# Kernel optimization log

Hardware: AMD Instinct MI355X
Metric: run time of the kernel (lower is better)

Reference implementation:

```python
import jax, jax.numpy as jnp
import numpy as np

IMG = 224; P = 16; C_IN = 3; D = 768; DEPTH = 12; H = 12; HD = D // H
MLP = 4 * D; NCLS = 1000
GRID = IMG // P; NPATCH = GRID * GRID; N = NPATCH + 1
NRD = (2 * GRID - 1) * (2 * GRID - 1) + 3  # num_relative_distance


def _rel_pos_index():
    # replicates the torch buffer construction (BEiT-style)
    coords = np.stack(np.meshgrid(np.arange(GRID), np.arange(GRID), indexing='ij')).reshape(2, -1)
    rel = (coords[:, :, None] - coords[:, None, :]).transpose(1, 2, 0).astype(np.int64)
    rel[:, :, 0] += GRID - 1
    rel[:, :, 1] += GRID - 1
    rel[:, :, 0] *= 2 * GRID - 1
    idx = np.zeros((N, N), dtype=np.int64)
    idx[1:, 1:] = rel.sum(-1)
    idx[0, :] = NRD - 3
    idx[:, 0] = NRD - 2
    idx[0, 0] = NRD - 1
    return jnp.asarray(idx)

REL_IDX = _rel_pos_index()  # [N, N] int


def setup_inputs() -> dict:
    key = jax.random.key(0)
    ks = jax.random.split(key, 12)
    r = lambda k, shp: jax.random.normal(k, shp, jnp.float32) * 0.02
    return {
        'x': jax.random.normal(ks[0], (32, C_IN, IMG, IMG), jnp.float32),
        'patch_w': r(ks[1], (D, C_IN * P * P)),
        'patch_b': jnp.zeros((D,), jnp.float32),
        'cls_token': r(ks[2], (1, 1, D)),
        'pos_embed': r(ks[3], (1, N, D)),
        'norm1_s': jnp.ones((DEPTH, D), jnp.float32),
        'norm1_b': jnp.zeros((DEPTH, D), jnp.float32),
        'qkv_w': r(ks[4], (DEPTH, 3 * D, D)),
        'q_bias': jnp.zeros((DEPTH, D), jnp.float32),
        'v_bias': jnp.zeros((DEPTH, D), jnp.float32),
        'rpb_table': r(ks[5], (DEPTH, NRD, H)),
        'proj_w': r(ks[6], (DEPTH, D, D)),
        'proj_b': jnp.zeros((DEPTH, D), jnp.float32),
        'norm2_s': jnp.ones((DEPTH, D), jnp.float32),
        'norm2_b': jnp.zeros((DEPTH, D), jnp.float32),
        'fc1_w': r(ks[7], (DEPTH, MLP, D)),
        'fc1_b': jnp.zeros((DEPTH, MLP), jnp.float32),
        'fc2_w': r(ks[8], (DEPTH, D, MLP)),
        'fc2_b': jnp.zeros((DEPTH, D), jnp.float32),
        'gamma1': jnp.full((DEPTH, D), 0.1, jnp.float32),
        'gamma2': jnp.full((DEPTH, D), 0.1, jnp.float32),
        'normf_s': jnp.ones((D,), jnp.float32),
        'normf_b': jnp.zeros((D,), jnp.float32),
        'head_w': r(ks[9], (NCLS, D)),
        'head_b': jnp.zeros((NCLS,), jnp.float32),
    }


def _ln(x, s, b):
    m = jnp.mean(x, -1, keepdims=True)
    v = jnp.mean((x - m) ** 2, -1, keepdims=True)
    return (x - m) * jax.lax.rsqrt(v + 1e-5) * s + b


def reference(x, patch_w, patch_b, cls_token, pos_embed, norm1_s, norm1_b, qkv_w,
              q_bias, v_bias, rpb_table, proj_w, proj_b, norm2_s, norm2_b,
              fc1_w, fc1_b, fc2_w, fc2_b, gamma1, gamma2, normf_s, normf_b,
              head_w, head_b):
    B = x.shape[0]
    # Patch embed: stride=kernel conv == unfold + matmul
    t = x.reshape(B, C_IN, GRID, P, GRID, P).transpose(0, 2, 4, 1, 3, 5).reshape(B, NPATCH, C_IN * P * P)
    t = t @ patch_w.T + patch_b                                   # [B, 196, D]
    t = jnp.concatenate([jnp.broadcast_to(cls_token, (B, 1, D)), t], axis=1) + pos_embed
    scale = HD ** -0.5
    for i in range(DEPTH):
        h = _ln(t, norm1_s[i], norm1_b[i])
        qkv_b = jnp.concatenate([q_bias[i], jnp.zeros_like(q_bias[i]), v_bias[i]])
        qkv = (h @ qkv_w[i].T + qkv_b).reshape(B, N, 3, H, HD)
        q = qkv[:, :, 0].transpose(0, 2, 1, 3)                    # [B, H, N, HD]
        k = qkv[:, :, 1].transpose(0, 2, 1, 3)
        v = qkv[:, :, 2].transpose(0, 2, 1, 3)
        bias = rpb_table[i][REL_IDX].transpose(2, 0, 1)           # [H, N, N]
        attn = jax.nn.softmax(jnp.einsum('bhqd,bhkd->bhqk', q * scale, k) + bias[None], axis=-1)
        o = jnp.einsum('bhqk,bhkd->bhqd', attn, v).transpose(0, 2, 1, 3).reshape(B, N, D)
        t = t + gamma1[i] * (o @ proj_w[i].T + proj_b[i])
        h2 = _ln(t, norm2_s[i], norm2_b[i])
        m = jax.nn.gelu(h2 @ fc1_w[i].T + fc1_b[i], approximate=False) @ fc2_w[i].T + fc2_b[i]
        t = t + gamma2[i] * m
    t = _ln(t, normf_s, normf_b)
    return t[:, 0] @ head_w.T + head_b                            # [B, NCLS]
```

## Files before the change

kernel.cpp:

```cpp
#include <hip/hip_runtime.h>
#include <hip/hip_bf16.h>


typedef __hip_bfloat16 bf16s;
using bf16x8 = __attribute__((ext_vector_type(8))) __bf16;
using f32x4  = __attribute__((ext_vector_type(4))) float;

#define DEV static __device__ __forceinline__

DEV float b2f(bf16s x) { return __bfloat162float(x); }
DEV bf16s f2b(float x) { return __float2bfloat16(x); }

DEV void gload_lds16(const void* g, void* l) {
  __builtin_amdgcn_global_load_lds((const __attribute__((address_space(1))) void*)g,
                                   (__attribute__((address_space(3))) void*)l, 16, 0, 0);
}

constexpr int B_   = 32;
constexpr int H_   = 12;
constexpr int NTOK = 197;
constexpr int NPAD = 224;
constexpr int MVALP= 6272;
constexpr int MVAL = B_*NTOK;
constexpr int MROW = 6400;
constexpr int MLP_ = 3072;
constexpr int BH   = B_*H_;
constexpr int NRD  = 732;
constexpr int NN   = NTOK*NTOK;

constexpr size_t OFF_T   = 0;
constexpr size_t SZ_T    = (size_t)MROW*768*4;
constexpr size_t OFF_H   = OFF_T + SZ_T;
constexpr size_t SZ_H    = (size_t)MROW*768*2;
constexpr size_t OFF_Q   = OFF_H + SZ_H;
constexpr size_t SZ_QKB  = (size_t)BH*NPAD*64*2;
constexpr size_t OFF_K   = OFF_Q + SZ_QKB;
constexpr size_t OFF_VT  = OFF_K + SZ_QKB;
constexpr size_t OFF_P   = OFF_VT + SZ_QKB;
constexpr size_t SZ_P    = (size_t)MROW*MLP_*2;
constexpr size_t OFF_O   = OFF_P + SZ_P;
constexpr size_t OFF_BT  = OFF_O + SZ_H;
constexpr size_t SZ_BT   = (size_t)12*H_*NN*2;
constexpr size_t OFF_HF  = OFF_BT + SZ_BT;
constexpr size_t OFF_WB  = OFF_HF + 49152;
constexpr size_t WS_NEED = OFF_WB + (size_t)7077888*2;

constexpr size_t WB_QKV = 0;
constexpr size_t WB_PROJ= (size_t)2304*768;
constexpr size_t WB_FC1 = WB_PROJ + (size_t)768*768;
constexpr size_t WB_FC2 = WB_FC1 + (size_t)MLP_*768;

template<int MODE>
__global__ __launch_bounds__(512, 4)
void gemm8p(const bf16s* __restrict__ A, const bf16s* __restrict__ Bw,
            const int K, const int ldc,
            bf16s* __restrict__ Cb,
            const float* __restrict__ e0, const float* __restrict__ e1,
            float* __restrict__ tres,
            bf16s* __restrict__ qp, bf16s* __restrict__ kp, bf16s* __restrict__ vp)
{
  __shared__ bf16s lds[32768];
  const int tid  = threadIdx.x;
  const int lane = tid & 63;
  const int wid  = tid >> 6;
  const int wm   = wid >> 2, wn = wid & 3;

  const int ncols = gridDim.y;
  const int nwg = (int)gridDim.x * ncols;
  const int lin = (int)blockIdx.y * gridDim.x + blockIdx.x;
  const int xcd = lin & 7, pos = lin >> 3;
  const int q8 = nwg >> 3, r8 = nwg & 7;
  const int vid = (xcd < r8) ? xcd*(q8+1) + pos : r8*(q8+1) + (xcd-r8)*q8 + pos;

  int bm, bn, koff = 0, ksl = 0;
  if (MODE == 6) {
    ksl = vid / 300;
    const int rem = vid - ksl*300;
    bm = rem / 6; bn = rem - bm*6;
    koff = ksl * 768;
  } else {
    constexpr int NBG = (MODE == 0) ? 6 : 8;
    const int gsz = NBG * (int)gridDim.x;
    const int g   = vid / gsz;
    const int rr  = vid - g*gsz;
    bm  = rr / NBG;
    bn  = g*NBG + (rr - bm*NBG);
  }

  const int ldk = (MODE == 6) ? ldc : K;
  const int srow = (wid << 3) + (lane >> 3);
  const int colg = ((lane & 7) << 3) ^ (((srow >> 2) & 1) << 4);
  const bf16s* gA = A  + (size_t)(bm*128 + srow)*ldk + koff + colg;
  const bf16s* gB = Bw + (size_t)(bn*128 + srow)*ldk + koff + colg;
  const size_t rK64 = (size_t)64*ldk;

  const int r15  = lane & 15;
  const int colr = (lane >> 4) << 3;
  const int cxor = ((lane >> 2) & 1) << 4;
  const int ardA = wm*4096 + r15*64;
  const int ardB = 8192 + (wn*32 + r15)*64;

  f32x4 acc[4][2] = {};
  const int J = K >> 7;

#define STGA(h, kt, dbuf) do { \
    const bf16s* _g = gA + (size_t)(h)*rK64 + (size_t)(kt)*64; \
    gload_lds16(_g, &lds[(dbuf)*16384 + (h)*4096 + wid*512 + lane*8]); } while(0)
#define STGB(h, kt, dbuf) do { \
    const bf16s* _g = gB + (size_t)(h)*rK64 + (size_t)(kt)*64; \
    gload_lds16(_g, &lds[(dbuf)*16384 + 8192 + (h)*4096 + wid*512 + lane*8]); } while(0)

  STGB(0,0,0); STGB(1,0,0);
  STGA(0,0,0); STGA(1,0,0);
  STGB(0,1,1); STGB(1,1,1);

  bf16x8 bfr[2][2];

  for (int j = 0; j < J; ++j) {
    const bool more = (j+1 < J);
#pragma unroll
    for (int p = 0; p < 4; ++p) {
      __builtin_amdgcn_sched_barrier(0);
      if (p == 0) {
        asm volatile("s_waitcnt vmcnt(2)" ::: "memory");
      } else if (p == 2) {
        if (j+1 == J) asm volatile("s_waitcnt vmcnt(0)" ::: "memory");
        else          asm volatile("s_waitcnt vmcnt(2)" ::: "memory");
      }
      __builtin_amdgcn_sched_barrier(0);
      __builtin_amdgcn_s_barrier();
      __builtin_amdgcn_sched_barrier(0);

      if (p == 0)      { STGA(0, 2*j+1, 1); STGA(1, 2*j+1, 1); }
      else if (p == 1) { if (more) { STGB(0, 2*j+2, 0); STGB(1, 2*j+2, 0); } }
      else if (p == 2) { if (more) { STGA(0, 2*j+2, 0); STGA(1, 2*j+2, 0); } }
      else             { if (more) { STGB(0, 2*j+3, 1); STGB(1, 2*j+3, 1); } }

      const int d = (p < 2) ? 0 : 1;
      const int dbase = d*16384;
      const int q0 = (p & 1) << 1;
      if ((p & 1) == 0) {
#pragma unroll
        for (int nf=0; nf<2; nf++)
#pragma unroll
          for (int kss=0; kss<2; kss++)
            bfr[nf][kss] = *(const bf16x8*)&lds[dbase + ardB + nf*1024 + (((kss<<5) + colr) ^ cxor)];
      }
      bf16x8 a1[2][2];
#pragma unroll
      for (int qq=0; qq<2; qq++)
#pragma unroll
        for (int kss=0; kss<2; kss++)
          a1[qq][kss] = *(const bf16x8*)&lds[dbase + ardA + (q0+qq)*1024 + (((kss<<5) + colr) ^ cxor)];
      __builtin_amdgcn_s_setprio(1);
#pragma unroll
      for (int qq=0; qq<2; qq++)
#pragma unroll
        for (int nf=0; nf<2; nf++)
#pragma unroll
          for (int kss=0; kss<2; kss++)
            acc[q0+qq][nf] = __builtin_amdgcn_mfma_f32_16x16x32_bf16(a1[qq][kss], bfr[nf][kss], acc[q0+qq][nf], 0, 0, 0);
      __builtin_amdgcn_s_setprio(0);
    }
  }
#undef STGA
#undef STGB

  const int crow0 = (lane >> 4) * 4;

  if (MODE == 6) {
#pragma unroll
    for (int mf = 0; mf < 4; ++mf) {
#pragma unroll
      for (int r = 0; r < 4; ++r) {
        const int grow = bm*128 + wm*64 + mf*16 + crow0 + r;
        float* trow = tres + (size_t)grow*768;
#pragma unroll
        for (int nf = 0; nf < 2; ++nf) {
          const int gcol = bn*128 + wn*32 + nf*16 + r15;
          const float add = e1[gcol]*(acc[mf][nf][r] + ((ksl == 0) ? e0[gcol] : 0.0f));
          unsafeAtomicAdd(&trow[gcol], add);
        }
      }
    }
    return;
  }

  if (MODE == 5) {
#pragma unroll
    for (int mf = 0; mf < 4; ++mf) {
#pragma unroll
      for (int r = 0; r < 4; ++r) {
        const int grow = bm*128 + wm*64 + mf*16 + crow0 + r;
        bf16s* crow = Cb + (size_t)grow*ldc;
#pragma unroll
        for (int nf = 0; nf < 2; ++nf) {
          const int gcol = bn*128 + wn*32 + nf*16 + r15;
          const float xx = acc[mf][nf][r] + e0[gcol];
          crow[gcol] = f2b(0.5f*xx*(1.0f + erff(xx*0.70710678118654752f)));
        }
      }
    }
    return;
  }

  if (MODE == 0 && bn >= 12) {
    float* lf = (float*)lds;
    __syncthreads();
#pragma unroll
    for (int mf = 0; mf < 4; ++mf)
#pragma unroll
      for (int nf = 0; nf < 2; ++nf)
#pragma unroll
        for (int r = 0; r < 4; ++r) {
          const int col = wn*32 + nf*16 + r15;
          const int row = wm*64 + mf*16 + crow0 + r;
          lf[col*128 + (row ^ (col & 31))] = acc[mf][nf][r];
        }
    __syncthreads();
    const int rem0 = bn*128 - 1536;
#pragma unroll
    for (int ci = 0; ci < 16; ++ci) {
      const int c = wid*16 + ci;
      const int rem = rem0 + c;
      const int hh = rem >> 6, dd = rem & 63;
      const float vb = e1[rem];
      bf16s* vrow = vp + ((size_t)hh*64 + dd)*NPAD;
#pragma unroll
      for (int hf2 = 0; hf2 < 2; ++hf2) {
        const int row = hf2*64 + lane;
        const int grow = bm*128 + row;
        if (grow < MVAL) {
          const int b2 = grow/197, ntok = grow - b2*197;
          vrow[(size_t)b2*H_*64*NPAD + ntok] = f2b(lf[c*128 + (row ^ (c & 31))] + vb);
        }
      }
    }
    return;
  }

  if (MODE == 0) {
#pragma unroll
    for (int mf = 0; mf < 4; ++mf) {
#pragma unroll
      for (int r = 0; r < 4; ++r) {
        const int grow = bm*128 + wm*64 + mf*16 + crow0 + r;
        if (grow >= MVAL) continue;
        const int bb_ = grow/197, ntok = grow - bb_*197;
#pragma unroll
        for (int nf = 0; nf < 2; ++nf) {
          const int gcol = bn*128 + wn*32 + nf*16 + r15;
          const float v = acc[mf][nf][r];
          const int rem = (gcol >= 768) ? gcol-768 : gcol;
          const int hh = rem >> 6, dd = rem & 63;
          const size_t bh = (size_t)bb_*H_ + hh;
          if (gcol < 768) qp[(bh*NPAD + ntok)*64 + dd] = f2b((v + e0[rem])*0.125f);
          else            kp[(bh*NPAD + ntok)*64 + dd] = f2b(v);
        }
      }
    }
  }
}

template<int MODE>
__global__ __launch_bounds__(256, 3)
void gemm64n(const bf16s* __restrict__ A, const bf16s* __restrict__ Bw,
             const int K, const int ldc, bf16s* __restrict__ Cb,
             const float* __restrict__ e0, const float* __restrict__ e1,
             float* __restrict__ tres)
{
  __shared__ bf16s lds[24576];
  const int tid  = threadIdx.x;
  const int lane = tid & 63;
  const int wid  = tid >> 6;
  const int wm   = wid >> 1, wn = wid & 1;

  const int ncols = gridDim.y;
  const int nwg = (int)gridDim.x * ncols;
  const int lin = (int)blockIdx.y * gridDim.x + blockIdx.x;
  const int xcd = lin & 7, pos = lin >> 3;
  const int q8 = nwg >> 3, r8 = nwg & 7;
  const int vid = (xcd < r8) ? xcd*(q8+1) + pos : r8*(q8+1) + (xcd-r8)*q8 + pos;
  const int bm = vid / ncols, bn = vid - bm*ncols;

  const int srow = tid >> 3;
  const int colg = ((tid & 7) << 3) ^ (((srow >> 2) & 1) << 4);
  const bf16s* gA = A  + (size_t)(bm*128 + srow)*K + colg;
  const bf16s* gB = Bw + (size_t)(bn*64  + srow)*K + colg;
  const size_t rK32 = (size_t)32*K;

  const int r15  = lane & 15;
  const int colr = (lane >> 4) << 3;
  const int cxor = ((lane >> 2) & 1) << 4;
  const int ardA = wm*4096 + r15*64;
  const int ardB = 8192 + (wn*32 + r15)*64;

  f32x4 acc[4][2] = {};
  const int J = K >> 7;

#define STGA2(h, kt, dbuf) do { \
    const bf16s* _g = gA + (size_t)(h)*rK32 + (size_t)(kt)*64; \
    gload_lds16(_g, &lds[(dbuf)*12288 + (h)*2048 + tid*8]); } while(0)
#define STGB2(h, kt, dbuf) do { \
    const bf16s* _g = gB + (size_t)(h)*rK32 + (size_t)(kt)*64; \
    gload_lds16(_g, &lds[(dbuf)*12288 + 8192 + (h)*2048 + tid*8]); } while(0)

  STGB2(0,0,0); STGB2(1,0,0);
  STGA2(0,0,0); STGA2(1,0,0); STGA2(2,0,0); STGA2(3,0,0);
  STGB2(0,1,1); STGB2(1,1,1);

  bf16x8 bfr[2][2];

  for (int j = 0; j < J; ++j) {
    const bool more = (j+1 < J);
#pragma unroll
    for (int p = 0; p < 4; ++p) {
      __builtin_amdgcn_sched_barrier(0);
      if (p == 0) {
        asm volatile("s_waitcnt vmcnt(2)" ::: "memory");
      } else if (p == 2) {
        if (j+1 == J) asm volatile("s_waitcnt vmcnt(0)" ::: "memory");
        else          asm volatile("s_waitcnt vmcnt(2)" ::: "memory");
      }
      __builtin_amdgcn_sched_barrier(0);
      __builtin_amdgcn_s_barrier();
      __builtin_amdgcn_sched_barrier(0);

      if (p == 0)      { STGA2(0, 2*j+1, 1); STGA2(1, 2*j+1, 1); STGA2(2, 2*j+1, 1); STGA2(3, 2*j+1, 1); }
      else if (p == 1) { if (more) { STGB2(0, 2*j+2, 0); STGB2(1, 2*j+2, 0); } }
      else if (p == 2) { if (more) { STGA2(0, 2*j+2, 0); STGA2(1, 2*j+2, 0); STGA2(2, 2*j+2, 0); STGA2(3, 2*j+2, 0); } }
      else             { if (more) { STGB2(0, 2*j+3, 1); STGB2(1, 2*j+3, 1); } }

      const int d = (p < 2) ? 0 : 1;
      const int dbase = d*12288;
      const int q0 = (p & 1) << 1;
      if ((p & 1) == 0) {
#pragma unroll
        for (int nf=0; nf<2; nf++)
#pragma unroll
          for (int kss=0; kss<2; kss++)
            bfr[nf][kss] = *(const bf16x8*)&lds[dbase + ardB + nf*1024 + (((kss<<5) + colr) ^ cxor)];
      }
      bf16x8 a1[2][2];
#pragma unroll
      for (int qq=0; qq<2; qq++)
#pragma unroll
        for (int kss=0; kss<2; kss++)
          a1[qq][kss] = *(const bf16x8*)&lds[dbase + ardA + (q0+qq)*1024 + (((kss<<5) + colr) ^ cxor)];
      __builtin_amdgcn_s_setprio(1);
#pragma unroll
      for (int qq=0; qq<2; qq++)
#pragma unroll
        for (int nf=0; nf<2; nf++)
#pragma unroll
          for (int kss=0; kss<2; kss++)
            acc[q0+qq][nf] = __builtin_amdgcn_mfma_f32_16x16x32_bf16(a1[qq][kss], bfr[nf][kss], acc[q0+qq][nf], 0, 0, 0);
      __builtin_amdgcn_s_setprio(0);
    }
  }
#undef STGA2
#undef STGB2

  const int crow0 = (lane >> 4) * 4;
#pragma unroll
  for (int mf = 0; mf < 4; ++mf) {
#pragma unroll
    for (int r = 0; r < 4; ++r) {
      const int grow = bm*128 + wm*64 + mf*16 + crow0 + r;
      if (MODE == 3) {
        bf16s* crow = Cb + (size_t)grow*ldc;
#pragma unroll
        for (int nf = 0; nf < 2; ++nf) {
          const int gcol = bn*64 + wn*32 + nf*16 + r15;
          const float xx = acc[mf][nf][r] + e0[gcol];
          crow[gcol] = f2b(0.5f*xx*(1.0f + erff(xx*0.70710678118654752f)));
        }
      } else {
        float* trow = tres + (size_t)grow*768;
#pragma unroll
        for (int nf = 0; nf < 2; ++nf) {
          const int gcol = bn*64 + wn*32 + nf*16 + r15;
          trow[gcol] += e1[gcol]*(acc[mf][nf][r] + e0[gcol]);
        }
      }
    }
  }
}

__global__ __launch_bounds__(256, 5)
void gemm64p(const bf16s* __restrict__ A, const bf16s* __restrict__ Bw,
             int K,
             const float* __restrict__ e0, const float* __restrict__ e1,
             float* __restrict__ tres)
{
  __shared__ bf16s As[2][64*32];
  __shared__ bf16s Bs[2][128*32];
  const int tid  = threadIdx.x;
  const int lane = tid & 63;
  const int wave = tid >> 6;

  const int ncols = gridDim.y;
  const int nwg = (int)gridDim.x * ncols;
  const int lin = (int)blockIdx.y * gridDim.x + blockIdx.x;
  const int xcd = lin & 7, pos = lin >> 3;
  const int q8 = nwg >> 3, r8 = nwg & 7;
  const int vid = (xcd < r8) ? xcd*(q8+1) + pos : r8*(q8+1) + (xcd-r8)*q8 + pos;
  const int bm = vid / ncols, bn = vid - bm*ncols;

  f32x4 acc[2][4] = {};

  const int sr4  = lane >> 2;
  const int scol = ((lane&3) ^ (sr4&3))*8;
  const bf16s* gA = A  + (size_t)(bm*64  + wave*16 + sr4)*K + scol;
  const bf16s* gB = Bw + (size_t)(bn*128 + wave*32 + sr4)*K + scol;
  const size_t b16 = (size_t)16*K;
  const int dA  = wave*512  + lane*8;
  const int dB0 = wave*1024 + lane*8, dB1 = dB0 + 512;

  const int fr  = lane & 15;
  const int rdk = (((lane>>4) ^ (lane&3)))*8;
  const int wr = wave >> 1, wc = wave & 1;
  const int abase = (wr*32 + fr)*32 + rdk;
  const int bbase = (wc*64 + fr)*32 + rdk;

  const int nk = K >> 5;
  gload_lds16(gA,       &As[0][dA]);
  gload_lds16(gB,       &Bs[0][dB0]);
  gload_lds16(gB + b16, &Bs[0][dB1]);

  int cur = 0;
  for (int kt = 0; kt < nk; ++kt) {
    __syncthreads();
    if (kt + 1 < nk) {
      const bf16s* ga = gA + (size_t)(kt+1)*32;
      const bf16s* gb = gB + (size_t)(kt+1)*32;
      gload_lds16(ga,       &As[cur^1][dA]);
      gload_lds16(gb,       &Bs[cur^1][dB0]);
      gload_lds16(gb + b16, &Bs[cur^1][dB1]);
    }
    bf16x8 af[2], bfr[4];
    af[0] = *(const bf16x8*)&As[cur][abase];
    af[1] = *(const bf16x8*)&As[cur][abase + 512];
#pragma unroll
    for (int n2=0;n2<4;n2++) bfr[n2] = *(const bf16x8*)&Bs[cur][bbase + n2*512];
#pragma unroll
    for (int m=0;m<2;m++)
#pragma unroll
      for (int n2=0;n2<4;n2++)
        acc[m][n2] = __builtin_amdgcn_mfma_f32_16x16x32_bf16(af[m], bfr[n2], acc[m][n2], 0, 0, 0);
    cur ^= 1;
  }

  const int crow0 = (lane>>4)*4;
#pragma unroll
  for (int m=0;m<2;m++) {
#pragma unroll
    for (int r=0;r<4;r++) {
      const int grow = bm*64 + wr*32 + m*16 + crow0 + r;
      if (grow >= MVALP) continue;
      const int bb_ = grow/196, p = grow - bb_*196;
      float* trow = tres + ((size_t)bb_*197 + 1 + p)*768;
      const float* prow = e1 + (size_t)(1+p)*768;
#pragma unroll
      for (int n2=0;n2<4;n2++) {
        const int gcol = bn*128 + wc*64 + n2*16 + fr;
        trow[gcol] = acc[m][n2][r] + e0[gcol] + prow[gcol];
      }
    }
  }
}

__global__ __launch_bounds__(256)
void f2b_k(const float* __restrict__ src, bf16s* __restrict__ dst, int n4)
{
  int id = blockIdx.x*256 + threadIdx.x;
  if (id >= n4) return;
  const float4 v = ((const float4*)src)[id];
  union { bf16s b[4]; uint2 u; } uu;
  uu.b[0] = f2b(v.x); uu.b[1] = f2b(v.y); uu.b[2] = f2b(v.z); uu.b[3] = f2b(v.w);
  ((uint2*)dst)[id] = uu.u;
}

__global__ __launch_bounds__(256)
void prep_k(const float* __restrict__ tin, const float* __restrict__ s,
            const float* __restrict__ b, bf16s* __restrict__ outp,
            const float* __restrict__ qw, const float* __restrict__ pw,
            const float* __restrict__ f1, const float* __restrict__ f2,
            bf16s* __restrict__ wb)
{
  const int tid = threadIdx.x;
  if (blockIdx.x < MVAL) {
    const int r = blockIdx.x;
    const float* xr = tin + (size_t)r*768;
    float v0 = xr[tid], v1 = xr[tid+256], v2 = xr[tid+512];
    float sum = v0+v1+v2;
#pragma unroll
    for (int off=32; off>=1; off>>=1) sum += __shfl_xor(sum, off, 64);
    __shared__ float red[8];
    const int wv = tid>>6, ln = tid&63;
    if (ln==0) red[wv] = sum;
    __syncthreads();
    const float mean = (red[0]+red[1]+red[2]+red[3]) * (1.0f/768.0f);
    const float d0=v0-mean, d1=v1-mean, d2=v2-mean;
    float sq = d0*d0 + d1*d1 + d2*d2;
#pragma unroll
    for (int off=32; off>=1; off>>=1) sq += __shfl_xor(sq, off, 64);
    if (ln==0) red[4+wv] = sq;
    __syncthreads();
    const float rs = rsqrtf((red[4]+red[5]+red[6]+red[7])*(1.0f/768.0f) + 1e-5f);
    bf16s* orow = outp + (size_t)r*768;
    orow[tid]     = f2b(d0*rs*s[tid]     + b[tid]);
    orow[tid+256] = f2b(d1*rs*s[tid+256] + b[tid+256]);
    orow[tid+512] = f2b(d2*rs*s[tid+512] + b[tid+512]);
  } else {
    int id = (blockIdx.x - MVAL)*256 + tid;
    const float* src; size_t dst; int loc;
    if (id < 442368)           { src = qw; loc = id;          dst = WB_QKV; }
    else if (id < 589824)      { src = pw; loc = id-442368;   dst = WB_PROJ; }
    else if (id < 1179648)     { src = f1; loc = id-589824;   dst = WB_FC1; }
    else                       { src = f2; loc = id-1179648;  dst = WB_FC2; }
    const float4 v = ((const float4*)src)[loc];
    union { bf16s bb[4]; uint2 u; } uu;
    uu.bb[0] = f2b(v.x); uu.bb[1] = f2b(v.y); uu.bb[2] = f2b(v.z); uu.bb[3] = f2b(v.w);
    ((uint2*)(wb + dst))[loc] = uu.u;
  }
}

__global__ __launch_bounds__(256)
void bias_all_k(const float* __restrict__ rpb, bf16s* __restrict__ biasT)
{
  int id = blockIdx.x*256 + threadIdx.x;
  if (id >= 12*H_*NN) return;
  const int l   = id / (H_*NN);
  const int r2  = id - l*(H_*NN);
  const int hh  = r2 / NN;
  const int rem = r2 - hh*NN;
  const int i = rem / 197, j = rem - i*197;
  int v;
  if (i==0 && j==0)      v = NRD-1;
  else if (i==0)         v = NRD-3;
  else if (j==0)         v = NRD-2;
  else {
    const int p = i-1, q = j-1;
    v = (p/14 - q/14 + 13)*27 + (p%14 - q%14 + 13);
  }
  biasT[id] = f2b(rpb[(size_t)l*NRD*H_ + v*H_ + hh]);
}

__global__ __launch_bounds__(256)
void im2col_k(const float* __restrict__ x, bf16s* __restrict__ pat)
{
  int id = blockIdx.x*256 + threadIdx.x;
  if (id >= MVALP*768) return;
  int col = id % 768;  int row = id / 768;
  int b = row / 196, p = row % 196;
  int gy = p / 14, gx = p % 14;
  int c = col >> 8, rem = col & 255, py = rem >> 4, px = rem & 15;
  pat[id] = f2b(x[ ((size_t)(b*3 + c)*224 + gy*16 + py)*224 + gx*16 + px ]);
}

__global__ __launch_bounds__(256)
void clspos_k(const float* __restrict__ cls, const float* __restrict__ pos, float* __restrict__ t)
{
  int id = blockIdx.x*256 + threadIdx.x;
  int d = id % 768, b = id / 768;
  t[(size_t)b*197*768 + d] = cls[d] + pos[d];
}

__global__ __launch_bounds__(256)
void ln_k(const float* __restrict__ tin, const float* __restrict__ s,
          const float* __restrict__ b, bf16s* __restrict__ outp, int instride)
{
  const int r = blockIdx.x, tid = threadIdx.x;
  const float* xr = tin + (size_t)r*instride;
  float v0 = xr[tid], v1 = xr[tid+256], v2 = xr[tid+512];
  float sum = v0+v1+v2;
#pragma unroll
  for (int off=32; off>=1; off>>=1) sum += __shfl_xor(sum, off, 64);
  __shared__ float red[8];
  const int wv = tid>>6, ln = tid&63;
  if (ln==0) red[wv] = sum;
  __syncthreads();
  const float mean = (red[0]+red[1]+red[2]+red[3]) * (1.0f/768.0f);
  const float d0=v0-mean, d1=v1-mean, d2=v2-mean;
  float sq = d0*d0 + d1*d1 + d2*d2;
#pragma unroll
  for (int off=32; off>=1; off>>=1) sq += __shfl_xor(sq, off, 64);
  if (ln==0) red[4+wv] = sq;
  __syncthreads();
  const float rs = rsqrtf((red[4]+red[5]+red[6]+red[7])*(1.0f/768.0f) + 1e-5f);
  bf16s* orow = outp + (size_t)r*768;
  orow[tid]     = f2b(d0*rs*s[tid]     + b[tid]);
  orow[tid+256] = f2b(d1*rs*s[tid+256] + b[tid+256]);
  orow[tid+512] = f2b(d2*rs*s[tid+512] + b[tid+512]);
}

__global__ __launch_bounds__(64)
void attn_fused(const bf16s* __restrict__ q, const bf16s* __restrict__ k,
                const bf16s* __restrict__ vT, const bf16s* __restrict__ biasT,
                bf16s* __restrict__ o)
{
  __shared__ bf16s Pl[32][232];
  const int gid = blockIdx.x;
  const int qt = gid % 7, bh = gid / 7;
  const int b = bh / H_, hh = bh % H_;
  const int lane = threadIdx.x;
  const int fr = lane & 15, fk = (lane>>4)*8;
  const bf16s* qp = q + (size_t)bh*NPAD*64;
  const bf16s* kp = k + (size_t)bh*NPAD*64;
  bf16x8 a[2][2];
#pragma unroll
  for (int m=0;m<2;m++)
#pragma unroll
    for (int kk=0;kk<2;kk++)
      a[m][kk] = *(const bf16x8*)&qp[(qt*32 + m*16 + fr)*64 + kk*32 + fk];

  f32x4 acc[2][14] = {};
#pragma unroll
  for (int nt=0; nt<14; nt++) {
    bf16x8 bb0 = *(const bf16x8*)&kp[(nt*16 + fr)*64 + fk];
    bf16x8 bb1 = *(const bf16x8*)&kp[(nt*16 + fr)*64 + 32 + fk];
    acc[0][nt] = __builtin_amdgcn_mfma_f32_16x16x32_bf16(a[0][0], bb0, acc[0][nt], 0,0,0);
    acc[0][nt] = __builtin_amdgcn_mfma_f32_16x16x32_bf16(a[0][1], bb1, acc[0][nt], 0,0,0);
    acc[1][nt] = __builtin_amdgcn_mfma_f32_16x16x32_bf16(a[1][0], bb0, acc[1][nt], 0,0,0);
    acc[1][nt] = __builtin_amdgcn_mfma_f32_16x16x32_bf16(a[1][1], bb1, acc[1][nt], 0,0,0);
  }

  const bf16s* bT = biasT + (size_t)hh*NN;
#pragma unroll
  for (int m=0;m<2;m++) {
#pragma unroll
    for (int r2=0;r2<4;r2++) {
      const int lrow = m*16 + (lane>>4)*4 + r2;
      const int row = qt*32 + lrow;
      if (row < NTOK) {
        const bf16s* br = bT + (size_t)row*197;
        float s[14]; float mx = -3.0e38f;
#pragma unroll
        for (int nt=0; nt<14; nt++) {
          const int col = nt*16 + fr;
          float v = acc[m][nt][r2] + ((col < NTOK) ? b2f(br[col]) : 0.0f);
          s[nt] = v;
          if (col < NTOK) mx = fmaxf(mx, v);
        }
        mx = fmaxf(mx, __shfl_xor(mx, 1, 64));
        mx = fmaxf(mx, __shfl_xor(mx, 2, 64));
        mx = fmaxf(mx, __shfl_xor(mx, 4, 64));
        mx = fmaxf(mx, __shfl_xor(mx, 8, 64));
        float sum = 0.f;
#pragma unroll
        for (int nt=0; nt<14; nt++) {
          const int col = nt*16 + fr;
          float p = (col < NTOK) ? __expf(s[nt]-mx) : 0.0f;
          s[nt] = p; sum += p;
        }
        sum += __shfl_xor(sum, 1, 64);
        sum += __shfl_xor(sum, 2, 64);
        sum += __shfl_xor(sum, 4, 64);
        sum += __shfl_xor(sum, 8, 64);
        const float inv = 1.0f / sum;
#pragma unroll
        for (int nt=0; nt<14; nt++)
          Pl[lrow][nt*16 + fr] = f2b(s[nt]*inv);
      } else {
#pragma unroll
        for (int nt=0; nt<14; nt++)
          Pl[lrow][nt*16 + fr] = f2b(0.0f);
      }
    }
  }

  __syncthreads();

  const bf16s* Vp = vT + (size_t)bh*64*NPAD;
  f32x4 pacc[2][4] = {};
  for (int kt=0; kt<7; kt++) {
    bf16x8 a0 = *(const bf16x8*)&Pl[fr][kt*32 + fk];
    bf16x8 a1 = *(const bf16x8*)&Pl[16 + fr][kt*32 + fk];
#pragma unroll
    for (int nf=0;nf<4;nf++) {
      bf16x8 bb = *(const bf16x8*)&Vp[(size_t)(nf*16 + fr)*NPAD + kt*32 + fk];
      pacc[0][nf] = __builtin_amdgcn_mfma_f32_16x16x32_bf16(a0, bb, pacc[0][nf], 0,0,0);
      pacc[1][nf] = __builtin_amdgcn_mfma_f32_16x16x32_bf16(a1, bb, pacc[1][nf], 0,0,0);
    }
  }

  __syncthreads();
#pragma unroll
  for (int m=0;m<2;m++)
#pragma unroll
    for (int nf=0;nf<4;nf++)
#pragma unroll
      for (int r2=0;r2<4;r2++)
        Pl[m*16 + (lane>>4)*4 + r2][nf*16 + fr] = f2b(pacc[m][nf][r2]);
  __syncthreads();
  bf16s* obase = o + ((size_t)b*NTOK + qt*32)*768 + hh*64;
#pragma unroll
  for (int it=0; it<8; ++it) {
    const int id = it*64 + lane;
    const int row = id >> 4, c4 = (id & 15)*4;
    if (qt*32 + row < NTOK) {
      union { bf16s bb[4]; uint2 u; } uu;
      uu.bb[0]=Pl[row][c4]; uu.bb[1]=Pl[row][c4+1]; uu.bb[2]=Pl[row][c4+2]; uu.bb[3]=Pl[row][c4+3];
      *(uint2*)&obase[(size_t)row*768 + c4] = uu.u;
    }
  }
}

__global__ __launch_bounds__(256)
void head_k(const bf16s* __restrict__ hf, const float* __restrict__ hw,
            const float* __restrict__ hb, float* __restrict__ outp)
{
  const int b = blockIdx.y;
  const int n = blockIdx.x*256 + threadIdx.x;
  __shared__ float xs[768];
  for (int i=threadIdx.x; i<768; i+=256) xs[i] = b2f(hf[b*768+i]);
  __syncthreads();
  if (n < 1000) {
    const float* wr = hw + (size_t)n*768;
    float acc2 = hb[n];
    for (int k2=0;k2<768;k2++) acc2 += xs[k2]*wr[k2];
    outp[b*1000 + n] = acc2;
  }
}

extern "C" void kernel_launch(void* const* d_in, const int* in_sizes, int n_in,
                              void* d_out, int out_size, void* d_ws, size_t ws_size,
                              hipStream_t stream)
{
  const float* x       = (const float*)d_in[0];
  const float* patch_w = (const float*)d_in[1];
  const float* patch_b = (const float*)d_in[2];
  const float* cls_tok = (const float*)d_in[3];
  const float* pos_emb = (const float*)d_in[4];
  const float* norm1_s = (const float*)d_in[5];
  const float* norm1_b = (const float*)d_in[6];
  const float* qkv_w   = (const float*)d_in[7];
  const float* q_bias  = (const float*)d_in[8];
  const float* v_bias  = (const float*)d_in[9];
  const float* rpb     = (const float*)d_in[10];
  const float* proj_w  = (const float*)d_in[11];
  const float* proj_b  = (const float*)d_in[12];
  const float* norm2_s = (const float*)d_in[13];
  const float* norm2_b = (const float*)d_in[14];
  const float* fc1_w   = (const float*)d_in[15];
  const float* fc1_b   = (const float*)d_in[16];
  const float* fc2_w   = (const float*)d_in[17];
  const float* fc2_b   = (const float*)d_in[18];
  const float* gamma1  = (const float*)d_in[19];
  const float* gamma2  = (const float*)d_in[20];
  const float* normf_s = (const float*)d_in[21];
  const float* normf_b = (const float*)d_in[22];
  const float* head_w  = (const float*)d_in[23];
  const float* head_b  = (const float*)d_in[24];
  float* out = (float*)d_out;

  char* w = (char*)d_ws;
  float* t    = (float*)(w + OFF_T);
  bf16s* h    = (bf16s*)(w + OFF_H);
  bf16s* qb   = (bf16s*)(w + OFF_Q);
  bf16s* kb   = (bf16s*)(w + OFF_K);
  bf16s* vT   = (bf16s*)(w + OFF_VT);
  bf16s* m1   = (bf16s*)(w + OFF_P);
  bf16s* pat  = (bf16s*)(w + OFF_P);
  bf16s* o    = (bf16s*)(w + OFF_O);
  bf16s* biasT= (bf16s*)(w + OFF_BT);
  bf16s* hf   = (bf16s*)(w + OFF_HF);
  bf16s* wb   = (bf16s*)(w + OFF_WB);
  (void)ws_size; (void)in_sizes; (void)n_in; (void)out_size; (void)WS_NEED;

  hipMemsetAsync(h  + (size_t)MVAL*768,  0, (size_t)(MROW-MVAL)*768*2,  stream);
  hipMemsetAsync(o  + (size_t)MVAL*768,  0, (size_t)(MROW-MVAL)*768*2,  stream);
  hipMemsetAsync(m1 + (size_t)MVAL*MLP_, 0, (size_t)(MROW-MVAL)*MLP_*2, stream);
  hipMemsetAsync(qb, 0, SZ_QKB, stream);
  hipMemsetAsync(kb, 0, SZ_QKB, stream);
  hipMemsetAsync(vT, 0, SZ_QKB, stream);

  bias_all_k<<<(12*H_*NN + 255)/256, 256, 0, stream>>>(rpb, biasT);
  im2col_k<<<(MVALP*768)/256, 256, 0, stream>>>(x, pat);
  clspos_k<<<96, 256, 0, stream>>>(cls_tok, pos_emb, t);
  f2b_k<<<(768*768/4)/256, 256, 0, stream>>>(patch_w, wb, 768*768/4);
  gemm64p<<<dim3(98,6), 256, 0, stream>>>(pat, wb, 768, patch_b, pos_emb, t);

  for (int l = 0; l < 12; ++l) {
    prep_k<<<MVAL + 6912, 256, 0, stream>>>(t, norm1_s + l*768, norm1_b + l*768, h,
                                            qkv_w + (size_t)l*2304*768, proj_w + (size_t)l*768*768,
                                            fc1_w + (size_t)l*MLP_*768, fc2_w + (size_t)l*768*MLP_, wb);
    gemm8p<0><<<dim3(50,18), 512, 0, stream>>>(h, wb + WB_QKV, 768, 2304, nullptr,
                                               q_bias + l*768, v_bias + l*768, nullptr,
                                               qb, kb, vT);
    attn_fused<<<BH*7, 64, 0, stream>>>(qb, kb, vT, biasT + (size_t)l*H_*NN, o);
    gemm64n<2><<<dim3(50,12), 256, 0, stream>>>(o, wb + WB_PROJ, 768, 0, nullptr,
                                                proj_b + l*768, gamma1 + l*768, t);
    ln_k<<<MVAL, 256, 0, stream>>>(t, norm2_s + l*768, norm2_b + l*768, h, 768);
    gemm8p<5><<<dim3(50,24), 512, 0, stream>>>(h, wb + WB_FC1, 768, MLP_, m1,
                                               fc1_b + l*MLP_, nullptr, nullptr,
                                               nullptr, nullptr, nullptr);
    gemm8p<6><<<dim3(50,24), 512, 0, stream>>>(m1, wb + WB_FC2, 768, MLP_, nullptr,
                                               fc2_b + l*768, gamma2 + l*768, t,
                                               nullptr, nullptr, nullptr);
  }

  ln_k<<<32, 256, 0, stream>>>(t, normf_s, normf_b, hf, 197*768);
  head_k<<<dim3(4,32), 256, 0, stream>>>(hf, head_w, head_b, out);
}
```

Before: 3.272 ms.

## Replace FC2 split-K atomics with partial buffers reduced in next LayerNorm

The FC2 split-K GEMM no longer does atomic adds into the residual stream. Each K-slice now writes plain fp32 partials into a 4-slice buffer, and the next layer's prep_k (or the final LayerNorm) sums the partials, applies bias and gamma2, and updates the residual. This removes atomic contention in the FC2 epilogue at the cost of extra global traffic for writing and reading four partial planes. Separately, the LDS XOR swizzle changes from a 1-bit pattern to a full 3-bit row-based swizzle to cut bank conflicts, and a dead MODE 3 epilogue branch is removed.

Measured after the change: 2.898 ms. 1.13x faster.

```diff
diff --git a/kernel.cpp b/kernel.cpp
--- a/kernel.cpp
+++ b/kernel.cpp
@@ -43,7 +43,12 @@
 constexpr size_t SZ_BT   = (size_t)12*H_*NN*2;
 constexpr size_t OFF_HF  = OFF_BT + SZ_BT;
 constexpr size_t OFF_WB  = OFF_HF + 49152;
-constexpr size_t WS_NEED = OFF_WB + (size_t)7077888*2;
+constexpr size_t SZ_WB   = (size_t)7077888*2;
+constexpr size_t OFF_PK  = OFF_WB + SZ_WB;
+constexpr size_t SZ_PK   = (size_t)4*MROW*768*4;
+constexpr size_t WS_NEED = OFF_PK + SZ_PK;
+
+constexpr size_t PST = (size_t)MROW*768;
 
 constexpr size_t WB_QKV = 0;
 constexpr size_t WB_PROJ= (size_t)2304*768;
@@ -89,14 +94,14 @@
 
   const int ldk = (MODE == 6) ? ldc : K;
   const int srow = (wid << 3) + (lane >> 3);
-  const int colg = ((lane & 7) << 3) ^ (((srow >> 2) & 1) << 4);
+  const int colg = (((lane & 7) ^ (srow & 7)) << 3);
   const bf16s* gA = A  + (size_t)(bm*128 + srow)*ldk + koff + colg;
   const bf16s* gB = Bw + (size_t)(bn*128 + srow)*ldk + koff + colg;
   const size_t rK64 = (size_t)64*ldk;
 
   const int r15  = lane & 15;
   const int colr = (lane >> 4) << 3;
-  const int cxor = ((lane >> 2) & 1) << 4;
+  const int exor = (lane & 7) << 3;
   const int ardA = wm*4096 + r15*64;
   const int ardB = 8192 + (wn*32 + r15)*64;
 
@@ -144,14 +149,14 @@
         for (int nf=0; nf<2; nf++)
 #pragma unroll
           for (int kss=0; kss<2; kss++)
-            bfr[nf][kss] = *(const bf16x8*)&lds[dbase + ardB + nf*1024 + (((kss<<5) + colr) ^ cxor)];
+            bfr[nf][kss] = *(const bf16x8*)&lds[dbase + ardB + nf*1024 + (((kss<<5) + colr) ^ exor)];
       }
       bf16x8 a1[2][2];
 #pragma unroll
       for (int qq=0; qq<2; qq++)
 #pragma unroll
         for (int kss=0; kss<2; kss++)
-          a1[qq][kss] = *(const bf16x8*)&lds[dbase + ardA + (q0+qq)*1024 + (((kss<<5) + colr) ^ cxor)];
+          a1[qq][kss] = *(const bf16x8*)&lds[dbase + ardA + (q0+qq)*1024 + (((kss<<5) + colr) ^ exor)];
       __builtin_amdgcn_s_setprio(1);
 #pragma unroll
       for (int qq=0; qq<2; qq++)
@@ -169,17 +174,17 @@
   const int crow0 = (lane >> 4) * 4;
 
   if (MODE == 6) {
+    float* pb = tres + (size_t)ksl*PST;
 #pragma unroll
     for (int mf = 0; mf < 4; ++mf) {
 #pragma unroll
       for (int r = 0; r < 4; ++r) {
         const int grow = bm*128 + wm*64 + mf*16 + crow0 + r;
-        float* trow = tres + (size_t)grow*768;
+        float* prow = pb + (size_t)grow*768;
 #pragma unroll
         for (int nf = 0; nf < 2; ++nf) {
           const int gcol = bn*128 + wn*32 + nf*16 + r15;
-          const float add = e1[gcol]*(acc[mf][nf][r] + ((ksl == 0) ? e0[gcol] : 0.0f));
-          unsafeAtomicAdd(&trow[gcol], add);
+          prow[gcol] = acc[mf][nf][r];
         }
       }
     }
@@ -284,14 +289,14 @@
   const int bm = vid / ncols, bn = vid - bm*ncols;
 
   const int srow = tid >> 3;
-  const int colg = ((tid & 7) << 3) ^ (((srow >> 2) & 1) << 4);
+  const int colg = (((tid & 7) ^ (srow & 7)) << 3);
   const bf16s* gA = A  + (size_t)(bm*128 + srow)*K + colg;
   const bf16s* gB = Bw + (size_t)(bn*64  + srow)*K + colg;
   const size_t rK32 = (size_t)32*K;
 
   const int r15  = lane & 15;
   const int colr = (lane >> 4) << 3;
-  const int cxor = ((lane >> 2) & 1) << 4;
+  const int exor = (lane & 7) << 3;
   const int ardA = wm*4096 + r15*64;
   const int ardB = 8192 + (wn*32 + r15)*64;
 
@@ -339,14 +344,14 @@
         for (int nf=0; nf<2; nf++)
 #pragma unroll
           for (int kss=0; kss<2; kss++)
-            bfr[nf][kss] = *(const bf16x8*)&lds[dbase + ardB + nf*1024 + (((kss<<5) + colr) ^ cxor)];
+            bfr[nf][kss] = *(const bf16x8*)&lds[dbase + ardB + nf*1024 + (((kss<<5) + colr) ^ exor)];
       }
       bf16x8 a1[2][2];
 #pragma unroll
       for (int qq=0; qq<2; qq++)
 #pragma unroll
         for (int kss=0; kss<2; kss++)
-          a1[qq][kss] = *(const bf16x8*)&lds[dbase + ardA + (q0+qq)*1024 + (((kss<<5) + colr) ^ cxor)];
+          a1[qq][kss] = *(const bf16x8*)&lds[dbase + ardA + (q0+qq)*1024 + (((kss<<5) + colr) ^ exor)];
       __builtin_amdgcn_s_setprio(1);
 #pragma unroll
       for (int qq=0; qq<2; qq++)
@@ -367,15 +372,7 @@
 #pragma unroll
     for (int r = 0; r < 4; ++r) {
       const int grow = bm*128 + wm*64 + mf*16 + crow0 + r;
-      if (MODE == 3) {
-        bf16s* crow = Cb + (size_t)grow*ldc;
-#pragma unroll
-        for (int nf = 0; nf < 2; ++nf) {
-          const int gcol = bn*64 + wn*32 + nf*16 + r15;
-          const float xx = acc[mf][nf][r] + e0[gcol];
-          crow[gcol] = f2b(0.5f*xx*(1.0f + erff(xx*0.70710678118654752f)));
-        }
-      } else {
+      {
         float* trow = tres + (size_t)grow*768;
 #pragma unroll
         for (int nf = 0; nf < 2; ++nf) {
@@ -482,17 +479,29 @@
 }
 
 __global__ __launch_bounds__(256)
-void prep_k(const float* __restrict__ tin, const float* __restrict__ s,
+void prep_k(float* __restrict__ tio, const float* __restrict__ s,
             const float* __restrict__ b, bf16s* __restrict__ outp,
             const float* __restrict__ qw, const float* __restrict__ pw,
             const float* __restrict__ f1, const float* __restrict__ f2,
-            bf16s* __restrict__ wb)
+            bf16s* __restrict__ wb,
+            const float* __restrict__ pk, const float* __restrict__ g2,
+            const float* __restrict__ b2)
 {
   const int tid = threadIdx.x;
   if (blockIdx.x < MVAL) {
     const int r = blockIdx.x;
-    const float* xr = tin + (size_t)r*768;
+    float* xr = tio + (size_t)r*768;
     float v0 = xr[tid], v1 = xr[tid+256], v2 = xr[tid+512];
+    if (pk) {
+      const size_t base = (size_t)r*768;
+      const float p0 = pk[base+tid]     + pk[PST+base+tid]     + pk[2*PST+base+tid]     + pk[3*PST+base+tid];
+      const float p1 = pk[base+tid+256] + pk[PST+base+tid+256] + pk[2*PST+base+tid+256] + pk[3*PST+base+tid+256];
+      const float p2 = pk[base+tid+512] + pk[PST+base+tid+512] + pk[2*PST+base+tid+512] + pk[3*PST+base+tid+512];
+      v0 += g2[tid]    *(p0 + b2[tid]);
+      v1 += g2[tid+256]*(p1 + b2[tid+256]);
+      v2 += g2[tid+512]*(p2 + b2[tid+512]);
+      xr[tid] = v0; xr[tid+256] = v1; xr[tid+512] = v2;
+    }
     float sum = v0+v1+v2;
 #pragma unroll
     for (int off=32; off>=1; off>>=1) sum += __shfl_xor(sum, off, 64);
@@ -569,11 +578,24 @@
 
 __global__ __launch_bounds__(256)
 void ln_k(const float* __restrict__ tin, const float* __restrict__ s,
-          const float* __restrict__ b, bf16s* __restrict__ outp, int instride)
+          const float* __restrict__ b, bf16s* __restrict__ outp, int instride,
+          const float* __restrict__ pk, const float* __restrict__ g2,
+          const float* __restrict__ b2)
 {
   const int r = blockIdx.x, tid = threadIdx.x;
   const float* xr = tin + (size_t)r*instride;
   float v0 = xr[tid], v1 = xr[tid+256], v2 = xr[tid+512];
+  if (pk) {
+    const size_t base = (size_t)r*(size_t)instride;
+    const size_t bp = (size_t)r*197*768;
+    const float p0 = pk[bp+tid]     + pk[PST+bp+tid]     + pk[2*PST+bp+tid]     + pk[3*PST+bp+tid];
+    const float p1 = pk[bp+tid+256] + pk[PST+bp+tid+256] + pk[2*PST+bp+tid+256] + pk[3*PST+bp+tid+256];
+    const float p2 = pk[bp+tid+512] + pk[PST+bp+tid+512] + pk[2*PST+bp+tid+512] + pk[3*PST+bp+tid+512];
+    v0 += g2[tid]    *(p0 + b2[tid]);
+    v1 += g2[tid+256]*(p1 + b2[tid+256]);
+    v2 += g2[tid+512]*(p2 + b2[tid+512]);
+    (void)base;
+  }
   float sum = v0+v1+v2;
 #pragma unroll
   for (int off=32; off>=1; off>>=1) sum += __shfl_xor(sum, off, 64);
@@ -767,6 +789,7 @@
   bf16s* biasT= (bf16s*)(w + OFF_BT);
   bf16s* hf   = (bf16s*)(w + OFF_HF);
   bf16s* wb   = (bf16s*)(w + OFF_WB);
+  float* pbuf = (float*)(w + OFF_PK);
   (void)ws_size; (void)in_sizes; (void)n_in; (void)out_size; (void)WS_NEED;
 
   hipMemsetAsync(h  + (size_t)MVAL*768,  0, (size_t)(MROW-MVAL)*768*2,  stream);
@@ -783,24 +806,30 @@
   gemm64p<<<dim3(98,6), 256, 0, stream>>>(pat, wb, 768, patch_b, pos_emb, t);
 
   for (int l = 0; l < 12; ++l) {
+    const float* pkin = (l > 0) ? pbuf : nullptr;
+    const float* g2in = (l > 0) ? gamma2 + (l-1)*768 : nullptr;
+    const float* b2in = (l > 0) ? fc2_b  + (l-1)*768 : nullptr;
     prep_k<<<MVAL + 6912, 256, 0, stream>>>(t, norm1_s + l*768, norm1_b + l*768, h,
                                             qkv_w + (size_t)l*2304*768, proj_w + (size_t)l*768*768,
-                                            fc1_w + (size_t)l*MLP_*768, fc2_w + (size_t)l*768*MLP_, wb);
+                                            fc1_w + (size_t)l*MLP_*768, fc2_w + (size_t)l*768*MLP_, wb,
+                                            pkin, g2in, b2in);
     gemm8p<0><<<dim3(50,18), 512, 0, stream>>>(h, wb + WB_QKV, 768, 2304, nullptr,
                                                q_bias + l*768, v_bias + l*768, nullptr,
                                                qb, kb, vT);
     attn_fused<<<BH*7, 64, 0, stream>>>(qb, kb, vT, biasT + (size_t)l*H_*NN, o);
     gemm64n<2><<<dim3(50,12), 256, 0, stream>>>(o, wb + WB_PROJ, 768, 0, nullptr,
                                                 proj_b + l*768, gamma1 + l*768, t);
-    ln_k<<<MVAL, 256, 0, stream>>>(t, norm2_s + l*768, norm2_b + l*768, h, 768);
+    ln_k<<<MVAL, 256, 0, stream>>>(t, norm2_s + l*768, norm2_b + l*768, h, 768,
+                                   nullptr, nullptr, nullptr);
     gemm8p<5><<<dim3(50,24), 512, 0, stream>>>(h, wb + WB_FC1, 768, MLP_, m1,
                                                fc1_b + l*MLP_, nullptr, nullptr,
                                                nullptr, nullptr, nullptr);
     gemm8p<6><<<dim3(50,24), 512, 0, stream>>>(m1, wb + WB_FC2, 768, MLP_, nullptr,
-                                               fc2_b + l*768, gamma2 + l*768, t,
+                                               nullptr, nullptr, pbuf,
                                                nullptr, nullptr, nullptr);
   }
 
-  ln_k<<<32, 256, 0, stream>>>(t, normf_s, normf_b, hf, 197*768);
+  ln_k<<<32, 256, 0, stream>>>(t, normf_s, normf_b, hf, 197*768,
+                               pbuf, gamma2 + 11*768, fc2_b + 11*768);
   head_k<<<dim3(4,32), 256, 0, stream>>>(hf, head_w, head_b, out);
 }
```
